# Kernel tuning notes

Measured on AMD Instinct MI355X. Metric: run time of the kernel, lower is better.

## Reference

```python
import jax, jax.numpy as jnp
import numpy as np

# CSV_Architecture_v2 layout (per frame, 130 floats):
#   hand 0 block: [0]=handedness label, [1]=handedness prob, [2:65]=21*3 coords
#   hand 1 block: [65]=handedness label, [66]=handedness prob, [67:130]=coords
POS0, PROB0 = 0, 1
POS1, PROB1 = 65, 66
HAND_LEN = 65
FRAME_LEN = 2 * HAND_LEN


def _build_swap_pattern():
    all_idxs = np.arange(FRAME_LEN)
    idxs_0 = np.arange(0, HAND_LEN)
    idxs_1 = np.arange(HAND_LEN, FRAME_LEN)
    all_idxs[idxs_0], all_idxs[idxs_1] = all_idxs[idxs_1].copy(), all_idxs[idxs_0].copy()
    return jnp.asarray(all_idxs, dtype=jnp.int32)


def setup_inputs() -> dict:
    key = jax.random.key(0)
    B, S = 256, 1024
    X = jax.random.normal(key, (B, S, FRAME_LEN), dtype=jnp.float32)
    return {"X": X, "swap_pattern": _build_swap_pattern()}


def reference(X, swap_pattern):
    # Per-frame handedness labels / probabilities.
    h0 = X[..., POS0]
    h1 = X[..., POS1]
    p0 = X[..., PROB0]
    p1 = X[..., PROB1]

    nan0 = jnp.isnan(h0)
    nan1 = jnp.isnan(h1)
    no_nan = jnp.logical_and(~nan0, ~nan1)

    one = jnp.float32(1.0)
    zero = jnp.float32(0.0)

    # skip1: hands already ordered (right label > left label)
    skip1 = h1 > h0
    # skip2: both predictions NaN -> no hands detected
    skip2 = jnp.logical_and(nan0, nan1)
    # skip3: only hand 1 present, labeled right (==1)
    skip3 = jnp.logical_and(nan0, h1 == one)
    # skip4: only hand 0 present, labeled left (==0)
    skip4 = jnp.logical_and(nan1, h0 == zero)
    eq = h0 == h1
    # skip5: both labeled left, position-0 hand has higher prob
    skip5 = no_nan & eq & (h0 == zero) & (p0 > p1)
    # skip6: both labeled right, position-1 hand has higher prob
    skip6 = no_nan & eq & (h0 == one) & (p0 < p1)

    skip = skip1 | skip2 | skip3 | skip4 | skip5 | skip6

    # Vectorized replacement of nested tf.map_fn: gather-permute the frame
    # representation where a swap is required.
    swapped = X[..., swap_pattern]  # [B, S, FRAME_LEN]
    return jnp.where(skip[..., None], X, swapped)
```

## Files before the change

### kernel.cpp

```cpp
#include <hip/hip_runtime.h>

constexpr int FRAME_LEN = 130;
constexpr int HALF      = 65;
constexpr int BLOCK     = 256;
constexpr int FPB       = 256;

__global__ __launch_bounds__(BLOCK)
void hand_sorter_kernel(const float* __restrict__ X, float* __restrict__ out,
                        int n_frames) {
    __shared__ unsigned char s_skip[FPB];
    const int t = threadIdx.x;
    const long long frame0 = (long long)blockIdx.x * FPB;

    {
        const long long f = frame0 + t;
        if (f < n_frames) {
            const float* fr = X + f * (long long)FRAME_LEN;
            const float h0 = fr[0];
            const float p0 = fr[1];
            const float h1 = fr[HALF];
            const float p1 = fr[HALF + 1];
            const bool nan0 = (h0 != h0);
            const bool nan1 = (h1 != h1);
            const bool no_nan = !nan0 && !nan1;
            const bool eq = (h0 == h1);
            const bool skip =
                (h1 > h0) ||
                (nan0 && nan1) ||
                (nan0 && (h1 == 1.0f)) ||
                (nan1 && (h0 == 0.0f)) ||
                (no_nan && eq && (h0 == 0.0f) && (p0 > p1)) ||
                (no_nan && eq && (h0 == 1.0f) && (p0 < p1));
            s_skip[t] = (unsigned char)skip;
        }
    }
    __syncthreads();

    const long long rem = n_frames - frame0;
    const int frames_here = rem < (long long)FPB ? (int)rem : FPB;
    const long long chunk_f = frame0 * (long long)FRAME_LEN;
    const float* __restrict__ Xc = X + chunk_f;
    float* __restrict__ Oc = out + chunk_f;

    int fl = t / HALF;
    int jj = t - fl * HALF;
    for (int k = 0; k < HALF; ++k) {
        const int m = t + k * BLOCK;
        if (fl < frames_here) {
            float2 v;
            if (s_skip[fl]) {
                v = *(const float2*)(Xc + 2 * m);
            } else {
                const float* fb = Xc + fl * FRAME_LEN;
                int j0 = 2 * jj + HALF;
                if (j0 >= FRAME_LEN) j0 -= FRAME_LEN;
                int j1 = j0 + 1;
                if (j1 >= FRAME_LEN) j1 -= FRAME_LEN;
                v.x = fb[j0];
                v.y = fb[j1];
            }
            *(float2*)(Oc + 2 * m) = v;
        }
        jj += BLOCK - 3 * HALF;
        fl += 3;
        if (jj >= HALF) { jj -= HALF; fl += 1; }
    }
}

extern "C" void kernel_launch(void* const* d_in, const int* in_sizes, int n_in,
                              void* d_out, int out_size, void* d_ws, size_t ws_size,
                              hipStream_t stream) {
    const float* X = (const float*)d_in[0];
    float* out = (float*)d_out;
    const int n_frames = in_sizes[0] / FRAME_LEN;
    const int n_blocks = (n_frames + FPB - 1) / FPB;
    hand_sorter_kernel<<<n_blocks, BLOCK, 0, stream>>>(X, out, n_frames);
}
```

Baseline: 270.5 us.

## Stage frame chunks in shared memory and write float4 outputs

Each block now loads a chunk of 32 frames into LDS with coalesced float4 reads, computes skip flags from LDS, then gathers the permuted output from LDS and writes float4 stores. This replaces scattered per-element global gathers for swapped frames and the separate global reads of handedness fields. It adds LDS traffic, a constant-multiply division by 130 per element, and smaller blocks with a higher occupancy hint. Since 32*130 is divisible by 4, chunk bases stay 16-byte aligned.

```diff
diff --git a/kernel.cpp b/kernel.cpp
--- a/kernel.cpp
+++ b/kernel.cpp
@@ -3,67 +3,83 @@
 constexpr int FRAME_LEN = 130;
 constexpr int HALF      = 65;
 constexpr int BLOCK     = 256;
-constexpr int FPB       = 256;
+constexpr int FPB       = 32;
+constexpr int CHUNK_F   = FPB * FRAME_LEN;
+constexpr int CHUNK_V4  = CHUNK_F / 4;
 
-__global__ __launch_bounds__(BLOCK)
+__device__ __forceinline__ int div130(int idx) {
+    return (int)(((unsigned)idx * 8067u) >> 20);
+}
+
+__global__ __launch_bounds__(BLOCK, 8)
 void hand_sorter_kernel(const float* __restrict__ X, float* __restrict__ out,
                         int n_frames) {
+    __shared__ float s_buf[CHUNK_F];
     __shared__ unsigned char s_skip[FPB];
+
     const int t = threadIdx.x;
     const long long frame0 = (long long)blockIdx.x * FPB;
+    const long long rem = (long long)n_frames - frame0;
+    const int frames_here = rem < (long long)FPB ? (int)rem : FPB;
+    const int nf = frames_here * FRAME_LEN;
+    const int n4 = (nf + 3) >> 2;
+    const long long base = frame0 * (long long)FRAME_LEN;
+    const float4* __restrict__ Xv = (const float4*)(X + base);
+    float4* __restrict__ Ov = (float4*)(out + base);
 
-    {
-        const long long f = frame0 + t;
-        if (f < n_frames) {
-            const float* fr = X + f * (long long)FRAME_LEN;
-            const float h0 = fr[0];
-            const float p0 = fr[1];
-            const float h1 = fr[HALF];
-            const float p1 = fr[HALF + 1];
-            const bool nan0 = (h0 != h0);
-            const bool nan1 = (h1 != h1);
-            const bool no_nan = !nan0 && !nan1;
-            const bool eq = (h0 == h1);
-            const bool skip =
-                (h1 > h0) ||
-                (nan0 && nan1) ||
-                (nan0 && (h1 == 1.0f)) ||
-                (nan1 && (h0 == 0.0f)) ||
-                (no_nan && eq && (h0 == 0.0f) && (p0 > p1)) ||
-                (no_nan && eq && (h0 == 1.0f) && (p0 < p1));
-            s_skip[t] = (unsigned char)skip;
-        }
+    for (int i = t; i < n4; i += BLOCK) {
+        *(float4*)(s_buf + 4 * i) = Xv[i];
     }
     __syncthreads();
 
-    const long long rem = n_frames - frame0;
-    const int frames_here = rem < (long long)FPB ? (int)rem : FPB;
-    const long long chunk_f = frame0 * (long long)FRAME_LEN;
-    const float* __restrict__ Xc = X + chunk_f;
-    float* __restrict__ Oc = out + chunk_f;
+    if (t < frames_here) {
+        const float* fr = s_buf + t * FRAME_LEN;
+        const float h0 = fr[0];
+        const float p0 = fr[1];
+        const float h1 = fr[HALF];
+        const float p1 = fr[HALF + 1];
+        const bool nan0 = (h0 != h0);
+        const bool nan1 = (h1 != h1);
+        const bool no_nan = !nan0 && !nan1;
+        const bool eq = (h0 == h1);
+        const bool skip =
+            (h1 > h0) ||
+            (nan0 && nan1) ||
+            (nan0 && (h1 == 1.0f)) ||
+            (nan1 && (h0 == 0.0f)) ||
+            (no_nan && eq && (h0 == 0.0f) && (p0 > p1)) ||
+            (no_nan && eq && (h0 == 1.0f) && (p0 < p1));
+        s_skip[t] = (unsigned char)skip;
+    }
+    __syncthreads();
 
-    int fl = t / HALF;
-    int jj = t - fl * HALF;
-    for (int k = 0; k < HALF; ++k) {
-        const int m = t + k * BLOCK;
-        if (fl < frames_here) {
-            float2 v;
-            if (s_skip[fl]) {
-                v = *(const float2*)(Xc + 2 * m);
-            } else {
-                const float* fb = Xc + fl * FRAME_LEN;
-                int j0 = 2 * jj + HALF;
-                if (j0 >= FRAME_LEN) j0 -= FRAME_LEN;
-                int j1 = j0 + 1;
-                if (j1 >= FRAME_LEN) j1 -= FRAME_LEN;
-                v.x = fb[j0];
-                v.y = fb[j1];
+    for (int i = t; i < n4; i += BLOCK) {
+        const int idx = 4 * i;
+        float4 v;
+        float* vp = (float*)&v;
+        if (idx + 3 < nf) {
+#pragma unroll
+            for (int e = 0; e < 4; ++e) {
+                const int ide = idx + e;
+                const int fl = div130(ide);
+                const int jj = ide - fl * FRAME_LEN;
+                int sj = jj + (s_skip[fl] ? 0 : HALF);
+                if (sj >= FRAME_LEN) sj -= FRAME_LEN;
+                vp[e] = s_buf[fl * FRAME_LEN + sj];
             }
-            *(float2*)(Oc + 2 * m) = v;
+            Ov[i] = v;
+        } else {
+            for (int e = 0; e < 4; ++e) {
+                const int ide = idx + e;
+                if (ide < nf) {
+                    const int fl = div130(ide);
+                    const int jj = ide - fl * FRAME_LEN;
+                    int sj = jj + (s_skip[fl] ? 0 : HALF);
+                    if (sj >= FRAME_LEN) sj -= FRAME_LEN;
+                    out[base + ide] = s_buf[fl * FRAME_LEN + sj];
+                }
+            }
         }
-        jj += BLOCK - 3 * HALF;
-        fl += 3;
-        if (jj >= HALF) { jj -= HALF; fl += 1; }
     }
 }
 
```

Measured after the change: 239.8 us. -11.4%, faster.
